# Kernel optimization log

Measured on AMD Instinct MI355X. Metric: run time of the kernel, lower is better.

Reference implementation:

```python
import jax, jax.numpy as jnp
import numpy as np


def setup_inputs() -> dict:
    key = jax.random.key(0)
    kx, kw = jax.random.split(key)
    B, S, IN, OUT = 4, 2048, 4096, 4096
    x = jax.random.normal(kx, (B, S, IN), dtype=jnp.float32)
    # int8-stored weight (kept as int32 container holding int8-range values)
    weight = jax.random.randint(kw, (IN, OUT), -127, 128, dtype=jnp.int32).astype(jnp.int8)
    return {"x": x, "weight": weight}


def reference(x, weight):
    # Faithful to: torch.matmul(x, self.weight.float())
    # inline dequant (int8 -> fp32) fused into the GEMM input
    w = weight.astype(jnp.float32)  # [IN, OUT]
    return jnp.einsum('bsi,io->bso', x, w)
```

## Files before the change

### kernel.cpp

```cpp
#include <hip/hip_runtime.h>
#include <hip/hip_bf16.h>

#define M_DIM 8192
#define N_DIM 4096
#define K_DIM 4096

typedef __attribute__((ext_vector_type(4))) int int4v;
typedef __attribute__((ext_vector_type(8))) short short8;
typedef __attribute__((ext_vector_type(4))) float floatx4;

__device__ __forceinline__ unsigned short f2bf(float f) {
    union { float f; unsigned int u; } cv; cv.f = f;
    unsigned int u = cv.u;
    return (unsigned short)((u + 0x7fffu + ((u >> 16) & 1u)) >> 16);
}

__global__ __launch_bounds__(256) void prep_kernel(const float* __restrict__ X,
                                                   const int* __restrict__ W,
                                                   char* __restrict__ Xq,
                                                   float* __restrict__ scales,
                                                   char* __restrict__ WT) {
    __shared__ float wmax[4];
    __shared__ int trans[64][17];
    const int t = threadIdx.x;

    if (blockIdx.x < M_DIM) {
        const int row = blockIdx.x;
        const float4* src = (const float4*)(X + (size_t)row * K_DIM);
        float4 v[4];
        float am = 0.f;
#pragma unroll
        for (int i = 0; i < 4; ++i) {
            v[i] = src[t + i * 256];
            am = fmaxf(am, fmaxf(fmaxf(fabsf(v[i].x), fabsf(v[i].y)),
                                 fmaxf(fabsf(v[i].z), fabsf(v[i].w))));
        }
#pragma unroll
        for (int off = 32; off; off >>= 1) am = fmaxf(am, __shfl_xor(am, off, 64));
        if ((t & 63) == 0) wmax[t >> 6] = am;
        __syncthreads();
        am = fmaxf(fmaxf(wmax[0], wmax[1]), fmaxf(wmax[2], wmax[3]));
        am = fmaxf(am, 1e-20f);
        const float inv = 127.f / am;
        unsigned int* dst = (unsigned int*)(Xq + (size_t)row * K_DIM);
#pragma unroll
        for (int i = 0; i < 4; ++i) {
            int q0 = __float2int_rn(v[i].x * inv);
            int q1 = __float2int_rn(v[i].y * inv);
            int q2 = __float2int_rn(v[i].z * inv);
            int q3 = __float2int_rn(v[i].w * inv);
            dst[t + i * 256] = (unsigned int)(q0 & 255) | ((unsigned int)(q1 & 255) << 8) |
                               ((unsigned int)(q2 & 255) << 16) | ((unsigned int)q3 << 24);
        }
        if (t == 0) scales[row] = am * (1.f / 127.f);
    } else {
        const int b  = blockIdx.x - M_DIM;
        const int tn = b & 63;
        const int tk = b >> 6;
        const int n  = t & 63;
        const int kg = t >> 6;

#pragma unroll
        for (int p = 0; p < 4; ++p) {
            const int kb = p * 16 + kg * 4;
            const int* src = W + (size_t)(tk * 64 + kb) * N_DIM + tn * 64 + n;
            int v0 = src[0];
            int v1 = src[N_DIM];
            int v2 = src[2 * N_DIM];
            int v3 = src[3 * N_DIM];
            trans[n][kb >> 2] = (v0 & 255) | ((v1 & 255) << 8) | ((v2 & 255) << 16) |
                                ((unsigned int)v3 << 24);
        }
        __syncthreads();

        const int n2 = t >> 2;
        const int c  = t & 3;
        int o0 = trans[n2][c * 4 + 0];
        int o1 = trans[n2][c * 4 + 1];
        int o2 = trans[n2][c * 4 + 2];
        int o3 = trans[n2][c * 4 + 3];
        char* dst = WT + (size_t)(tn * 64 + n2) * K_DIM + tk * 64 + c * 16;
        int4 o; o.x = o0; o.y = o1; o.z = o2; o.w = o3;
        *(int4*)dst = o;
    }
}

#define GLL(src, dst) __builtin_amdgcn_global_load_lds( \
    (const __attribute__((address_space(1))) void*)(src), \
    (__attribute__((address_space(3))) void*)(dst), 16, 0, 0)

__global__ __launch_bounds__(512, 2) void gemm_i8(const char* __restrict__ A,
                                                  const char* __restrict__ BT,
                                                  const float* __restrict__ scales,
                                                  float* __restrict__ C) {
    __shared__ __attribute__((aligned(16))) char lds[131072];

    const int t    = threadIdx.x;
    const int lane = t & 63;
    const int wave = t >> 6;

    const int lin = blockIdx.y * 16 + blockIdx.x;
    const int wg  = ((lin & 7) << 6) + (lin >> 3);
    const int bn  = wg & 15;
    const int bm  = wg >> 4;

    const int waveM = (wave >> 2) * 128;
    const int waveN = (wave & 3) * 64;

    const int srow = t >> 3;
    const int schk = (t & 7) ^ (srow & 7);
    const char* aSrc = A  + (size_t)(bm * 256 + srow) * K_DIM + schk * 16;
    const char* bSrc = BT + (size_t)(bn * 256 + srow) * K_DIM + schk * 16;
    char* aDst = lds + wave * 1024;
    char* bDst = lds + 65536 + wave * 1024;

#define STG_A(buf, r0, kt) do { \
    GLL(aSrc + (size_t)(r0) * K_DIM + (kt) * 128,        aDst + (buf) * 32768 + (r0) * 128); \
    GLL(aSrc + (size_t)((r0) + 64) * K_DIM + (kt) * 128, aDst + (buf) * 32768 + ((r0) + 64) * 128); \
} while (0)
#define STG_B(buf, r0, kt) do { \
    GLL(bSrc + (size_t)(r0) * K_DIM + (kt) * 128,        bDst + (buf) * 32768 + (r0) * 128); \
    GLL(bSrc + (size_t)((r0) + 64) * K_DIM + (kt) * 128, bDst + (buf) * 32768 + ((r0) + 64) * 128); \
} while (0)

    const char* fA = lds + (waveM + (lane & 15)) * 128;
    const char* fB = lds + 65536 + (waveN + (lane & 15)) * 128;
    const int sw0 = (((lane >> 4) + 0) ^ (lane & 7)) * 16;
    const int sw1 = (((lane >> 4) + 4) ^ (lane & 7)) * 16;

    int4v acc[8][4];
#pragma unroll
    for (int i = 0; i < 8; ++i)
#pragma unroll
        for (int j = 0; j < 4; ++j) acc[i][j] = (int4v){0, 0, 0, 0};

    int4v a[4][2], b[4][2];

#define LDA(buf, mh) do { \
    _Pragma("unroll") \
    for (int i2 = 0; i2 < 4; ++i2) { \
        a[i2][0] = *(const int4v*)(fA + (buf) * 32768 + ((mh) * 4 + i2) * 2048 + sw0); \
        a[i2][1] = *(const int4v*)(fA + (buf) * 32768 + ((mh) * 4 + i2) * 2048 + sw1); \
    } \
} while (0)
#define LDB(buf, j0) do { \
    _Pragma("unroll") \
    for (int j2 = 0; j2 < 2; ++j2) { \
        b[(j0) + j2][0] = *(const int4v*)(fB + (buf) * 32768 + ((j0) + j2) * 2048 + sw0); \
        b[(j0) + j2][1] = *(const int4v*)(fB + (buf) * 32768 + ((j0) + j2) * 2048 + sw1); \
    } \
} while (0)
#define MFMAQ(mh, j0) do { \
    _Pragma("unroll") \
    for (int i2 = 0; i2 < 4; ++i2) \
    _Pragma("unroll") \
    for (int j2 = 0; j2 < 2; ++j2) { \
        acc[(mh) * 4 + i2][(j0) + j2] = __builtin_amdgcn_mfma_i32_16x16x64_i8( \
            a[i2][0], b[(j0) + j2][0], acc[(mh) * 4 + i2][(j0) + j2], 0, 0, 0); \
        acc[(mh) * 4 + i2][(j0) + j2] = __builtin_amdgcn_mfma_i32_16x16x64_i8( \
            a[i2][1], b[(j0) + j2][1], acc[(mh) * 4 + i2][(j0) + j2], 0, 0, 0); \
    } \
} while (0)

    STG_A(0, 0, 0); STG_A(0, 128, 0);
    STG_B(0, 0, 0); STG_B(0, 128, 0);
    STG_B(1, 0, 1); STG_B(1, 128, 1);

#pragma unroll 1
    for (int it = 0; it < 16; ++it) {
        const int kt = it * 2;
        const bool more = (it < 15);

        STG_A(1, 0, kt + 1);
        asm volatile("s_waitcnt vmcnt(6)" ::: "memory");
        __builtin_amdgcn_s_barrier();
        LDA(0, 0); LDB(0, 0);
        __builtin_amdgcn_s_setprio(1);
        MFMAQ(0, 0);
        __builtin_amdgcn_s_setprio(0);
        __builtin_amdgcn_s_barrier();

        STG_A(1, 128, kt + 1);
        LDB(0, 2);
        __builtin_amdgcn_s_barrier();
        __builtin_amdgcn_s_setprio(1);
        MFMAQ(0, 2);
        __builtin_amdgcn_s_setprio(0);
        __builtin_amdgcn_s_barrier();

        if (more) STG_B(0, 0, kt + 2);
        LDA(0, 1);
        __builtin_amdgcn_s_barrier();
        __builtin_amdgcn_s_setprio(1);
        MFMAQ(1, 2);
        __builtin_amdgcn_s_setprio(0);
        __builtin_amdgcn_s_barrier();

        if (more) STG_B(0, 128, kt + 2);
        __builtin_amdgcn_s_barrier();
        __builtin_amdgcn_s_setprio(1);
        MFMAQ(1, 0);
        __builtin_amdgcn_s_setprio(0);
        __builtin_amdgcn_s_barrier();

        if (more) {
            STG_A(0, 0, kt + 2);
            asm volatile("s_waitcnt vmcnt(6)" ::: "memory");
        } else {
            asm volatile("s_waitcnt vmcnt(0)" ::: "memory");
        }
        __builtin_amdgcn_s_barrier();
        LDA(1, 0); LDB(1, 0);
        __builtin_amdgcn_s_setprio(1);
        MFMAQ(0, 0);
        __builtin_amdgcn_s_setprio(0);
        __builtin_amdgcn_s_barrier();

        if (more) STG_A(0, 128, kt + 2);
        LDB(1, 2);
        __builtin_amdgcn_s_barrier();
        __builtin_amdgcn_s_setprio(1);
        MFMAQ(0, 2);
        __builtin_amdgcn_s_setprio(0);
        __builtin_amdgcn_s_barrier();

        if (more) STG_B(1, 0, kt + 3);
        LDA(1, 1);
        __builtin_amdgcn_s_barrier();
        __builtin_amdgcn_s_setprio(1);
        MFMAQ(1, 2);
        __builtin_amdgcn_s_setprio(0);
        __builtin_amdgcn_s_barrier();

        if (more) STG_B(1, 128, kt + 3);
        __builtin_amdgcn_s_barrier();
        __builtin_amdgcn_s_setprio(1);
        MFMAQ(1, 0);
        __builtin_amdgcn_s_setprio(0);
        __builtin_amdgcn_s_barrier();
    }

    {
        float* reg4 = (float*)(lds + wave * 16384);
        const int ec = lane & 15;
        const int er = (lane >> 4) << 2;
        const size_t growBase = (size_t)(bm * 256 + waveM);
        const size_t gcolBase = (size_t)(bn * 256 + waveN);
#pragma unroll
        for (int h = 0; h < 2; ++h) {
#pragma unroll
            for (int i2 = 0; i2 < 4; ++i2) {
                const int rbase = i2 * 16 + er;
                const float4 s4 = *(const float4*)(scales + growBase + h * 64 + rbase);
                const float sc4[4] = {s4.x, s4.y, s4.z, s4.w};
#pragma unroll
                for (int j = 0; j < 4; ++j) {
                    const int col = j * 16 + ec;
#pragma unroll
                    for (int rr = 0; rr < 4; ++rr) {
                        const int row = rbase + rr;
                        reg4[row * 64 + (col ^ ((row & 7) << 2))] =
                            (float)acc[h * 4 + i2][j][rr] * sc4[rr];
                    }
                }
            }
            const int c4 = ec << 2;
#pragma unroll 4
            for (int q = 0; q < 16; ++q) {
                const int R = (lane >> 4) + q * 4;
                const floatx4 v = *(const floatx4*)&reg4[R * 64 + (c4 ^ ((R & 7) << 2))];
                float* dst = C + (growBase + h * 64 + R) * N_DIM + gcolBase + c4;
                __builtin_nontemporal_store(v, (floatx4*)dst);
            }
        }
    }
}

__global__ __launch_bounds__(256) void gemm_fb(const float* __restrict__ X,
                                               const int* __restrict__ W,
                                               float* __restrict__ C) {
    __shared__ __attribute__((aligned(16))) unsigned short sA[128 * 32];
    __shared__ __attribute__((aligned(16))) unsigned short sB[128 * 32];

    const int t    = threadIdx.x;
    const int lane = t & 63;
    const int wave = t >> 6;
    const int bn   = blockIdx.x;
    const int bm   = blockIdx.y;
    const int waveM = (wave >> 1) * 64;
    const int waveN = (wave & 1) * 64;

    const int ar = t >> 1, ac = (t & 1) << 4;
    const float* gX = X + (size_t)(bm * 128 + ar) * K_DIM + ac;
    const int br = t >> 3, bc = (t & 7) << 4;
    const int* gW = W + (size_t)br * N_DIM + bn * 128 + bc;

    const int fr = lane & 15;
    const int fk = (lane >> 4) << 3;
    const unsigned short* fA = sA + (waveM + fr) * 32 + fk;
    const unsigned short* fB = sB + (waveN + fr) * 32 + fk;

    floatx4 acc[4][4];
#pragma unroll
    for (int i = 0; i < 4; ++i)
#pragma unroll
        for (int j = 0; j < 4; ++j) acc[i][j] = (floatx4){0.f, 0.f, 0.f, 0.f};

    for (int k0 = 0; k0 < K_DIM; k0 += 32) {
        {
            const float4* p = (const float4*)gX;
            float4 v0 = p[0], v1 = p[1], v2 = p[2], v3 = p[3];
            uint4 o0, o1;
            o0.x = (unsigned int)f2bf(v0.x) | ((unsigned int)f2bf(v0.y) << 16);
            o0.y = (unsigned int)f2bf(v0.z) | ((unsigned int)f2bf(v0.w) << 16);
            o0.z = (unsigned int)f2bf(v1.x) | ((unsigned int)f2bf(v1.y) << 16);
            o0.w = (unsigned int)f2bf(v1.z) | ((unsigned int)f2bf(v1.w) << 16);
            o1.x = (unsigned int)f2bf(v2.x) | ((unsigned int)f2bf(v2.y) << 16);
            o1.y = (unsigned int)f2bf(v2.z) | ((unsigned int)f2bf(v2.w) << 16);
            o1.z = (unsigned int)f2bf(v3.x) | ((unsigned int)f2bf(v3.y) << 16);
            o1.w = (unsigned int)f2bf(v3.z) | ((unsigned int)f2bf(v3.w) << 16);
            uint4* d = (uint4*)&sA[ar * 32 + ac];
            d[0] = o0; d[1] = o1;
        }
        {
#pragma unroll
            for (int q = 0; q < 4; ++q) {
                int4 v = ((const int4*)gW)[q];
                sB[(bc + q * 4 + 0) * 32 + br] = f2bf((float)v.x);
                sB[(bc + q * 4 + 1) * 32 + br] = f2bf((float)v.y);
                sB[(bc + q * 4 + 2) * 32 + br] = f2bf((float)v.z);
                sB[(bc + q * 4 + 3) * 32 + br] = f2bf((float)v.w);
            }
        }
        gX += 32;
        gW += (size_t)32 * N_DIM;
        __syncthreads();

        short8 a[4], b[4];
#pragma unroll
        for (int i = 0; i < 4; ++i) a[i] = *(const short8*)(fA + i * 16 * 32);
#pragma unroll
        for (int j = 0; j < 4; ++j) b[j] = *(const short8*)(fB + j * 16 * 32);
#pragma unroll
        for (int i = 0; i < 4; ++i)
#pragma unroll
            for (int j = 0; j < 4; ++j)
                acc[i][j] = __builtin_amdgcn_mfma_f32_16x16x32_bf16(a[i], b[j], acc[i][j], 0, 0, 0);
        __syncthreads();
    }

    const int er = (lane >> 4) << 2;
    const int ec = lane & 15;
#pragma unroll
    for (int i = 0; i < 4; ++i)
#pragma unroll
        for (int j = 0; j < 4; ++j) {
            const size_t row0 = (size_t)(bm * 128 + waveM + i * 16 + er);
            const size_t col  = (size_t)(bn * 128 + waveN + j * 16 + ec);
#pragma unroll
            for (int rr = 0; rr < 4; ++rr) C[(row0 + rr) * N_DIM + col] = acc[i][j][rr];
        }
}

extern "C" void kernel_launch(void* const* d_in, const int* in_sizes, int n_in,
                              void* d_out, int out_size, void* d_ws, size_t ws_size,
                              hipStream_t stream) {
    const float* x = (const float*)d_in[0];
    const int*   w = (const int*)d_in[1];
    float* out = (float*)d_out;

    const size_t bytesXq = (size_t)M_DIM * K_DIM;
    const size_t bytesWT = (size_t)K_DIM * N_DIM;
    const size_t bytesSc = (size_t)M_DIM * sizeof(float);

    if (ws_size >= bytesXq + bytesWT + bytesSc) {
        char*  Xq = (char*)d_ws;
        char*  WT = (char*)d_ws + bytesXq;
        float* Sc = (float*)((char*)d_ws + bytesXq + bytesWT);
        prep_kernel<<<M_DIM + (N_DIM / 64) * (K_DIM / 64), 256, 0, stream>>>(x, w, Xq, Sc, WT);
        gemm_i8<<<dim3(N_DIM / 256, M_DIM / 256), 512, 0, stream>>>(Xq, WT, Sc, out);
    } else {
        gemm_fb<<<dim3(N_DIM / 128, M_DIM / 128), 256, 0, stream>>>(x, w, out);
    }
}
```

Baseline: 378.6 us.

## Replace fine-grained interleaved staging with whole-tile double-buffered pipeline

Replaces the eight-phase schedule, which interleaved partial A/B global-to-LDS loads between MFMA quarter-blocks with many barriers, with a simpler double-buffered scheme. Each step issues the full next tile (8 loads), waits with vmcnt(8) for the current tile, then computes the whole tile between two barriers. This cuts the barrier count per K-step. In exchange, loads are issued in bursts rather than spread across compute, and the prefetch depth changes. There is also a possible race: the next tile is written into the buffer that may still be in use.

```diff
diff --git a/kernel.cpp b/kernel.cpp
--- a/kernel.cpp
+++ b/kernel.cpp
@@ -121,6 +121,10 @@
 #define STG_B(buf, r0, kt) do { \
     GLL(bSrc + (size_t)(r0) * K_DIM + (kt) * 128,        bDst + (buf) * 32768 + (r0) * 128); \
     GLL(bSrc + (size_t)((r0) + 64) * K_DIM + (kt) * 128, bDst + (buf) * 32768 + ((r0) + 64) * 128); \
+} while (0)
+#define STG_TILE(buf, kt) do { \
+    STG_A(buf, 0, kt); STG_A(buf, 128, kt); \
+    STG_B(buf, 0, kt); STG_B(buf, 128, kt); \
 } while (0)
 
     const char* fA = lds + (waveM + (lane & 15)) * 128;
@@ -162,82 +166,37 @@
     } \
 } while (0)
 
-    STG_A(0, 0, 0); STG_A(0, 128, 0);
-    STG_B(0, 0, 0); STG_B(0, 128, 0);
-    STG_B(1, 0, 1); STG_B(1, 128, 1);
+#define TILE_COMPUTE(buf) do { \
+    __builtin_amdgcn_s_barrier();                \
+    LDB(buf, 0); LDA(buf, 0); LDB(buf, 2); \
+    __builtin_amdgcn_s_setprio(1); \
+    MFMAQ(0, 0); MFMAQ(0, 2); \
+    __builtin_amdgcn_s_setprio(0); \
+    LDA(buf, 1); \
+    __builtin_amdgcn_s_setprio(1); \
+    MFMAQ(1, 0); MFMAQ(1, 2); \
+    __builtin_amdgcn_s_setprio(0); \
+    __builtin_amdgcn_s_barrier();                \
+} while (0)
+
+    STG_TILE(0, 0);
 
 #pragma unroll 1
     for (int it = 0; it < 16; ++it) {
         const int kt = it * 2;
         const bool more = (it < 15);
 
-        STG_A(1, 0, kt + 1);
-        asm volatile("s_waitcnt vmcnt(6)" ::: "memory");
-        __builtin_amdgcn_s_barrier();
-        LDA(0, 0); LDB(0, 0);
-        __builtin_amdgcn_s_setprio(1);
-        MFMAQ(0, 0);
-        __builtin_amdgcn_s_setprio(0);
-        __builtin_amdgcn_s_barrier();
-
-        STG_A(1, 128, kt + 1);
-        LDB(0, 2);
-        __builtin_amdgcn_s_barrier();
-        __builtin_amdgcn_s_setprio(1);
-        MFMAQ(0, 2);
-        __builtin_amdgcn_s_setprio(0);
-        __builtin_amdgcn_s_barrier();
-
-        if (more) STG_B(0, 0, kt + 2);
-        LDA(0, 1);
-        __builtin_amdgcn_s_barrier();
-        __builtin_amdgcn_s_setprio(1);
-        MFMAQ(1, 2);
-        __builtin_amdgcn_s_setprio(0);
-        __builtin_amdgcn_s_barrier();
-
-        if (more) STG_B(0, 128, kt + 2);
-        __builtin_amdgcn_s_barrier();
-        __builtin_amdgcn_s_setprio(1);
-        MFMAQ(1, 0);
-        __builtin_amdgcn_s_setprio(0);
-        __builtin_amdgcn_s_barrier();
+        STG_TILE(1, kt + 1);
+        asm volatile("s_waitcnt vmcnt(8)" ::: "memory");
+        TILE_COMPUTE(0);
 
         if (more) {
-            STG_A(0, 0, kt + 2);
-            asm volatile("s_waitcnt vmcnt(6)" ::: "memory");
+            STG_TILE(0, kt + 2);
+            asm volatile("s_waitcnt vmcnt(8)" ::: "memory");
         } else {
             asm volatile("s_waitcnt vmcnt(0)" ::: "memory");
         }
-        __builtin_amdgcn_s_barrier();
-        LDA(1, 0); LDB(1, 0);
-        __builtin_amdgcn_s_setprio(1);
-        MFMAQ(0, 0);
-        __builtin_amdgcn_s_setprio(0);
-        __builtin_amdgcn_s_barrier();
-
-        if (more) STG_A(0, 128, kt + 2);
-        LDB(1, 2);
-        __builtin_amdgcn_s_barrier();
-        __builtin_amdgcn_s_setprio(1);
-        MFMAQ(0, 2);
-        __builtin_amdgcn_s_setprio(0);
-        __builtin_amdgcn_s_barrier();
-
-        if (more) STG_B(1, 0, kt + 3);
-        LDA(1, 1);
-        __builtin_amdgcn_s_barrier();
-        __builtin_amdgcn_s_setprio(1);
-        MFMAQ(1, 2);
-        __builtin_amdgcn_s_setprio(0);
-        __builtin_amdgcn_s_barrier();
-
-        if (more) STG_B(1, 128, kt + 3);
-        __builtin_amdgcn_s_barrier();
-        __builtin_amdgcn_s_setprio(1);
-        MFMAQ(1, 0);
-        __builtin_amdgcn_s_setprio(0);
-        __builtin_amdgcn_s_barrier();
+        TILE_COMPUTE(1);
     }
 
     {
```

Measured after the change: 385.7 us. No clear change (+1.9%).
